# Kernel tuning notes

Measured on AMD Instinct MI355X. Metric: run time of the kernel, lower is better.

## Reference

```python
import jax, jax.numpy as jnp
import numpy as np

IN_F, OUT_F = 4096, 11008
MAXQ = 15  # 2**4 - 1 for wbits=4


def setup_inputs() -> dict:
    key = jax.random.key(0)
    k1, k2, k3, k4, k5 = jax.random.split(key, 5)
    inp = jax.random.normal(k1, (4, 64, IN_F), dtype=jnp.float32)
    weight = jax.random.normal(k2, (OUT_F, IN_F), dtype=jnp.float32) * 0.02
    bias = jax.random.normal(k3, (OUT_F,), dtype=jnp.float32) * 0.02
    # per-channel asymmetric quant params (as Quantizer.find_params would produce)
    scale = jax.random.uniform(k4, (OUT_F, 1), dtype=jnp.float32) * 0.01 + 1e-4
    zero = jnp.round(jax.random.uniform(k5, (OUT_F, 1), dtype=jnp.float32) * MAXQ)
    return {"input": inp, "weight": weight, "bias": bias,
            "scale": scale, "zero": zero, "maxq": MAXQ}


def reference(input, weight, bias, scale, zero, maxq):
    # fake-quantize weight: q = clamp(round(w/scale) + zero, 0, maxq); w_dq = scale*(q - zero)
    q = jnp.clip(jnp.round(weight / scale) + zero, 0.0, float(maxq))
    w_dq = scale * (q - zero)                      # [out, in]
    # F.linear: input @ w_dq.T + bias
    out = jnp.einsum('bsi,oi->bso', input, w_dq) + bias
    return out
```

## Files before the change

kernel.cpp:

```cpp
#include <hip/hip_runtime.h>
#include <stdint.h>

#define K_TOT 4096
#define N_TOT 11008
#define M_TOT 256
#define BM 128
#define BN 64
#define WST 72

using bf16x8 = __attribute__((ext_vector_type(8))) short;
using f32x4  = __attribute__((ext_vector_type(4))) float;

#define BAR() do {                                          \
    asm volatile("s_waitcnt lgkmcnt(0)" ::: "memory");      \
    __builtin_amdgcn_s_barrier();                           \
    asm volatile("" ::: "memory");                          \
} while (0)

__global__ void cvt_a_bf16(const float* __restrict__ in, uint32_t* __restrict__ out) {
    int i = blockIdx.x * blockDim.x + threadIdx.x;
    const float4 v = ((const float4*)in)[i];
    uint32_t a = __float_as_uint(v.x), b = __float_as_uint(v.y),
             c = __float_as_uint(v.z), d = __float_as_uint(v.w);
    a += 0x7FFFu + ((a >> 16) & 1u);
    b += 0x7FFFu + ((b >> 16) & 1u);
    c += 0x7FFFu + ((c >> 16) & 1u);
    d += 0x7FFFu + ((d >> 16) & 1u);
    uint2 o;
    o.x = (a >> 16) | (b & 0xFFFF0000u);
    o.y = (c >> 16) | (d & 0xFFFF0000u);
    ((uint2*)out)[i] = o;
}

__device__ __forceinline__ uint32_t pack_hi16(uint32_t u0, uint32_t u1) {
#if __has_builtin(__builtin_amdgcn_perm)
    return __builtin_amdgcn_perm(u1, u0, 0x07060302u);
#else
    return (u0 >> 16) | (u1 & 0xFFFF0000u);
#endif
}

__device__ __forceinline__ float clamp3(float q, float lo, float hi) {
#if __has_builtin(__builtin_amdgcn_fmed3f)
    return __builtin_amdgcn_fmed3f(q, lo, hi);
#else
    return fminf(fmaxf(q, lo), hi);
#endif
}

__device__ __forceinline__ void dequant16(const f32x4* w, float rs, float lo, float hi,
                                          float sc, uint32_t o[8]) {
    uint32_t u[16];
#pragma unroll
    for (int j = 0; j < 4; ++j) {
#pragma unroll
        for (int e = 0; e < 4; ++e) {
            float q  = rintf(w[j][e] * rs);
            q        = clamp3(q, lo, hi);
            float dq = q * sc;
            uint32_t b = __float_as_uint(dq);
            u[4 * j + e] = b + 0x7FFFu + ((b >> 16) & 1u);
        }
    }
#pragma unroll
    for (int i = 0; i < 8; ++i) o[i] = pack_hi16(u[2 * i], u[2 * i + 1]);
}

__global__ __launch_bounds__(256, 3)
void wql_gemm(const uint16_t* __restrict__ A,
              const float* __restrict__ W,
              const float* __restrict__ scale,
              const float* __restrict__ zero,
              float* __restrict__ P,
              int kloc) {
    __shared__ uint16_t sW[2][BN][WST];

    const int tid  = threadIdx.x;
    const int lane = tid & 63;
    const int wv   = tid >> 6;
    const int wm   = (wv & 1) * 64;
    const int wn   = (wv >> 1) * 32;
    const int m0   = blockIdx.x * BM;
    const int n0   = blockIdx.y * BN;
    const int k0   = blockIdx.z * kloc;
    const int nkt  = kloc >> 6;

    const int nloc = tid >> 2;
    const int kseg = tid & 3;
    const int wrow = n0 + nloc;
    const float* Wp = W + (size_t)wrow * K_TOT + k0 + kseg * 16;
    const float sc = scale[wrow];
    const float zp = zero[wrow];
    const float rs = 1.0f / sc;
    const float lo = -zp, hi = 15.0f - zp;

    const uint16_t* Ap[4];
#pragma unroll
    for (int mi = 0; mi < 4; ++mi)
        Ap[mi] = A + (size_t)(m0 + wm + mi * 16 + (lane & 15)) * K_TOT + k0 + (lane >> 4) * 8;

    f32x4 acc[4][2];
#pragma unroll
    for (int mi = 0; mi < 4; ++mi)
#pragma unroll
        for (int ni = 0; ni < 2; ++ni)
            acc[mi][ni] = (f32x4){0.f, 0.f, 0.f, 0.f};

    f32x4 bank[4][4];

#pragma unroll
    for (int s = 0; s < 3; ++s) {
        const f32x4* p = (const f32x4*)(Wp + (size_t)s * 64);
#pragma unroll
        for (int j = 0; j < 4; ++j) bank[s][j] = __builtin_nontemporal_load(p + j);
    }
    {
        uint32_t o[8];
        dequant16(bank[0], rs, lo, hi, sc, o);
        uint16_t* d = &sW[0][nloc][kseg * 16];
        ((uint4*)d)[0] = make_uint4(o[0], o[1], o[2], o[3]);
        ((uint4*)d)[1] = make_uint4(o[4], o[5], o[6], o[7]);
    }
    BAR();

    for (int st = 0; st < nkt; st += 4) {
#pragma unroll
        for (int u = 0; u < 4; ++u) {
            const int step = st + u;

            if (step + 3 < nkt) {
                const f32x4* p = (const f32x4*)(Wp + (size_t)(step + 3) * 64);
#pragma unroll
                for (int j = 0; j < 4; ++j)
                    bank[(u + 3) & 3][j] = __builtin_nontemporal_load(p + j);
            }

            {
                const int koff = step * 64;
#pragma unroll
                for (int s = 0; s < 2; ++s) {
                    bf16x8 a[4], b[2];
#pragma unroll
                    for (int mi = 0; mi < 4; ++mi)
                        a[mi] = *(const bf16x8*)(Ap[mi] + koff + s * 32);
#pragma unroll
                    for (int ni = 0; ni < 2; ++ni)
                        b[ni] = *(const bf16x8*)&sW[u & 1][wn + ni * 16 + (lane & 15)]
                                                  [s * 32 + (lane >> 4) * 8];
#pragma unroll
                    for (int mi = 0; mi < 4; ++mi)
#pragma unroll
                        for (int ni = 0; ni < 2; ++ni)
                            acc[mi][ni] = __builtin_amdgcn_mfma_f32_16x16x32_bf16(
                                a[mi], b[ni], acc[mi][ni], 0, 0, 0);
                }
            }

            if (step + 1 < nkt) {
                uint32_t o[8];
                dequant16(bank[(u + 1) & 3], rs, lo, hi, sc, o);
                uint16_t* d = &sW[(u + 1) & 1][nloc][kseg * 16];
                ((uint4*)d)[0] = make_uint4(o[0], o[1], o[2], o[3]);
                ((uint4*)d)[1] = make_uint4(o[4], o[5], o[6], o[7]);
            }

            BAR();
        }
    }

    float* Pb = P + (size_t)blockIdx.z * M_TOT * N_TOT;
    const int colbase = n0 + wn + (lane & 15);
    const int rbase = m0 + wm + ((lane >> 4) << 2);
#pragma unroll
    for (int mi = 0; mi < 4; ++mi) {
#pragma unroll
        for (int ni = 0; ni < 2; ++ni) {
            const int col = colbase + ni * 16;
#pragma unroll
            for (int r = 0; r < 4; ++r) {
                const int row = rbase + mi * 16 + r;
                __builtin_nontemporal_store(acc[mi][ni][r], &Pb[(size_t)row * N_TOT + col]);
            }
        }
    }
}

__global__ void reduce_bias(const float* __restrict__ P, const float* __restrict__ bias,
                            float* __restrict__ out, int ks) {
    const int i4 = blockIdx.x * blockDim.x + threadIdx.x;
    const size_t tot4 = (size_t)M_TOT * N_TOT / 4;
    const int col = (int)(((size_t)i4 * 4) % N_TOT);
    f32x4 acc = __builtin_nontemporal_load((const f32x4*)P + i4);
    for (int s = 1; s < ks; ++s) {
        const f32x4 v = __builtin_nontemporal_load((const f32x4*)P + (size_t)s * tot4 + i4);
        acc += v;
    }
    const float4 b = *(const float4*)(bias + col);
    acc[0] += b.x; acc[1] += b.y; acc[2] += b.z; acc[3] += b.w;
    *((f32x4*)out + i4) = acc;
}

extern "C" void kernel_launch(void* const* d_in, const int* in_sizes, int n_in,
                              void* d_out, int out_size, void* d_ws, size_t ws_size,
                              hipStream_t stream) {
    const float* inp    = (const float*)d_in[0];
    const float* weight = (const float*)d_in[1];
    const float* bias   = (const float*)d_in[2];
    const float* scale  = (const float*)d_in[3];
    const float* zero   = (const float*)d_in[4];

    const size_t A_BYTES = (size_t)M_TOT * K_TOT * 2;
    const size_t SLICE   = (size_t)M_TOT * N_TOT * 4;

    uint32_t* Abf = (uint32_t*)d_ws;
    float* partial;
    int KS;
    if (ws_size >= A_BYTES + 4 * SLICE) { KS = 4; partial = (float*)((char*)d_ws + A_BYTES); }
    else if (ws_size >= A_BYTES + 2 * SLICE) { KS = 2; partial = (float*)((char*)d_ws + A_BYTES); }
    else { KS = 1; partial = (float*)d_out; }

    cvt_a_bf16<<<dim3((M_TOT * K_TOT / 4) / 256), dim3(256), 0, stream>>>(inp, Abf);

    dim3 grid(M_TOT / BM, N_TOT / BN, KS);
    wql_gemm<<<grid, dim3(256), 0, stream>>>((const uint16_t*)Abf, weight, scale, zero,
                                             partial, K_TOT / KS);

    reduce_bias<<<dim3((M_TOT * N_TOT / 4) / 256), dim3(256), 0, stream>>>(
        partial, bias, (float*)d_out, KS);
}
```

Baseline: 407.7 us.

## Double-buffer A fragments in registers and drop nontemporal loads/stores

Prefetches the next k-step's bf16 A fragments into a double-buffered register array ahead of the MFMA loop, using sched_barrier to keep the prefetch ordered before compute. Weight bank loads, partial-sum stores and reduce loads switch from nontemporal to ordinary accesses, which may let the partials stay in cache between the GEMM and the reduction. This raises register pressure (an extra 16 bf16x8 registers) and could hurt occupancy at the 3-blocks-per-CU launch bound.

Result: slower. 435.9 us (+6.9%).

```diff
diff --git a/kernel.cpp b/kernel.cpp
--- a/kernel.cpp
+++ b/kernel.cpp
@@ -106,21 +106,31 @@
         for (int ni = 0; ni < 2; ++ni)
             acc[mi][ni] = (f32x4){0.f, 0.f, 0.f, 0.f};
 
-    f32x4 bank[4][4];
-
-#pragma unroll
-    for (int s = 0; s < 3; ++s) {
-        const f32x4* p = (const f32x4*)(Wp + (size_t)s * 64);
-#pragma unroll
-        for (int j = 0; j < 4; ++j) bank[s][j] = __builtin_nontemporal_load(p + j);
-    }
+    f32x4  bank[4][4];
+    bf16x8 ar[2][4][2];
+
     {
+        const f32x4* p = (const f32x4*)Wp;
+#pragma unroll
+        for (int j = 0; j < 4; ++j) bank[0][j] = p[j];
         uint32_t o[8];
         dequant16(bank[0], rs, lo, hi, sc, o);
         uint16_t* d = &sW[0][nloc][kseg * 16];
         ((uint4*)d)[0] = make_uint4(o[0], o[1], o[2], o[3]);
         ((uint4*)d)[1] = make_uint4(o[4], o[5], o[6], o[7]);
     }
+#pragma unroll
+    for (int mi = 0; mi < 4; ++mi)
+#pragma unroll
+        for (int s = 0; s < 2; ++s)
+            ar[0][mi][s] = *(const bf16x8*)(Ap[mi] + s * 32);
+    __builtin_amdgcn_sched_barrier(0);
+#pragma unroll
+    for (int ps = 1; ps <= 2; ++ps) {
+        const f32x4* p = (const f32x4*)(Wp + (size_t)ps * 64);
+#pragma unroll
+        for (int j = 0; j < 4; ++j) bank[ps][j] = p[j];
+    }
     BAR();
 
     for (int st = 0; st < nkt; st += 4) {
@@ -128,21 +138,27 @@
         for (int u = 0; u < 4; ++u) {
             const int step = st + u;
 
+            if (step + 1 < nkt) {
+                const int koff = (step + 1) * 64;
+#pragma unroll
+                for (int mi = 0; mi < 4; ++mi)
+#pragma unroll
+                    for (int s = 0; s < 2; ++s)
+                        ar[(u + 1) & 1][mi][s] = *(const bf16x8*)(Ap[mi] + koff + s * 32);
+            }
+            __builtin_amdgcn_sched_barrier(0);
+
             if (step + 3 < nkt) {
                 const f32x4* p = (const f32x4*)(Wp + (size_t)(step + 3) * 64);
 #pragma unroll
-                for (int j = 0; j < 4; ++j)
-                    bank[(u + 3) & 3][j] = __builtin_nontemporal_load(p + j);
-            }
+                for (int j = 0; j < 4; ++j) bank[(u + 3) & 3][j] = p[j];
+            }
+            __builtin_amdgcn_sched_barrier(0);
 
             {
-                const int koff = step * 64;
 #pragma unroll
                 for (int s = 0; s < 2; ++s) {
-                    bf16x8 a[4], b[2];
-#pragma unroll
-                    for (int mi = 0; mi < 4; ++mi)
-                        a[mi] = *(const bf16x8*)(Ap[mi] + koff + s * 32);
+                    bf16x8 b[2];
 #pragma unroll
                     for (int ni = 0; ni < 2; ++ni)
                         b[ni] = *(const bf16x8*)&sW[u & 1][wn + ni * 16 + (lane & 15)]
@@ -152,7 +168,7 @@
 #pragma unroll
                         for (int ni = 0; ni < 2; ++ni)
                             acc[mi][ni] = __builtin_amdgcn_mfma_f32_16x16x32_bf16(
-                                a[mi], b[ni], acc[mi][ni], 0, 0, 0);
+                                ar[u & 1][mi][s], b[ni], acc[mi][ni], 0, 0, 0);
                 }
             }
 
@@ -179,7 +195,7 @@
 #pragma unroll
             for (int r = 0; r < 4; ++r) {
                 const int row = rbase + mi * 16 + r;
-                __builtin_nontemporal_store(acc[mi][ni][r], &Pb[(size_t)row * N_TOT + col]);
+                Pb[(size_t)row * N_TOT + col] = acc[mi][ni][r];
             }
         }
     }
@@ -190,14 +206,14 @@
     const int i4 = blockIdx.x * blockDim.x + threadIdx.x;
     const size_t tot4 = (size_t)M_TOT * N_TOT / 4;
     const int col = (int)(((size_t)i4 * 4) % N_TOT);
-    f32x4 acc = __builtin_nontemporal_load((const f32x4*)P + i4);
+    float4 acc = ((const float4*)P)[i4];
     for (int s = 1; s < ks; ++s) {
-        const f32x4 v = __builtin_nontemporal_load((const f32x4*)P + (size_t)s * tot4 + i4);
-        acc += v;
+        const float4 v = ((const float4*)P)[(size_t)s * tot4 + i4];
+        acc.x += v.x; acc.y += v.y; acc.z += v.z; acc.w += v.w;
     }
     const float4 b = *(const float4*)(bias + col);
-    acc[0] += b.x; acc[1] += b.y; acc[2] += b.z; acc[3] += b.w;
-    *((f32x4*)out + i4) = acc;
+    acc.x += b.x; acc.y += b.y; acc.z += b.z; acc.w += b.w;
+    ((float4*)out)[i4] = acc;
 }
 
 extern "C" void kernel_launch(void* const* d_in, const int* in_sizes, int n_in,
```

## Restructure GEMM main loop with two-bank weight prefetch and sched barriers

Applied to the files above, without the earlier changes.

Reworks the main loop from a 4-deep register bank of weight prefetches into a 2-bank ping-pong macro with explicit sched_barriers. All A-fragment loads are hoisted ahead of the weight prefetch, and the MFMA order is interleaved with the B LDS reads. Nontemporal loads and stores are also replaced with ordinary ones in the GEMM epilogue and the reduction. The goal is lower register pressure and a more controlled instruction order, at the cost of a shallower prefetch distance that may expose more global load latency.

Result: faster. 340.4 us (-16.5%).

```diff
diff --git a/kernel.cpp b/kernel.cpp
--- a/kernel.cpp
+++ b/kernel.cpp
@@ -16,6 +16,8 @@
     __builtin_amdgcn_s_barrier();                           \
     asm volatile("" ::: "memory");                          \
 } while (0)
+
+#define MFMA(A, B, C) __builtin_amdgcn_mfma_f32_16x16x32_bf16((A), (B), (C), 0, 0, 0)
 
 __global__ void cvt_a_bf16(const float* __restrict__ in, uint32_t* __restrict__ out) {
     int i = blockIdx.x * blockDim.x + threadIdx.x;
@@ -66,6 +68,59 @@
     for (int i = 0; i < 8; ++i) o[i] = pack_hi16(u[2 * i], u[2 * i + 1]);
 }
 
+#define ITER(STEP, CUR, NXT, P) do {                                            \
+    const int _s = (STEP);                                                      \
+    const int _koff = _s * 64;                                                  \
+              \
+    bf16x8 a0 = *(const bf16x8*)(Ap0 + _koff),                                  \
+           a1 = *(const bf16x8*)(Ap0 + _koff + 32),                             \
+           a2 = *(const bf16x8*)(Ap1 + _koff),                                  \
+           a3 = *(const bf16x8*)(Ap1 + _koff + 32),                             \
+           a4 = *(const bf16x8*)(Ap2 + _koff),                                  \
+           a5 = *(const bf16x8*)(Ap2 + _koff + 32),                             \
+           a6 = *(const bf16x8*)(Ap3 + _koff),                                  \
+           a7 = *(const bf16x8*)(Ap3 + _koff + 32);                             \
+    __builtin_amdgcn_sched_barrier(0);                                          \
+     \
+    if (_s + 2 < nkt) {                                                         \
+        const f32x4* _p = (const f32x4*)(Wp + (size_t)(_s + 2) * 64);           \
+        CUR[0] = _p[0]; CUR[1] = _p[1]; CUR[2] = _p[2]; CUR[3] = _p[3];         \
+    }                                                                           \
+    __builtin_amdgcn_sched_barrier(0);                                          \
+                                    \
+    {                                                                           \
+        bf16x8 b00 = *(const bf16x8*)&sW[P][wn +      (lane & 15)][(lane >> 4) * 8]; \
+        bf16x8 b01 = *(const bf16x8*)&sW[P][wn + 16 + (lane & 15)][(lane >> 4) * 8]; \
+        acc[0][0] = MFMA(a0, b00, acc[0][0]);                                   \
+        acc[0][1] = MFMA(a0, b01, acc[0][1]);                                   \
+        acc[1][0] = MFMA(a2, b00, acc[1][0]);                                   \
+        acc[1][1] = MFMA(a2, b01, acc[1][1]);                                   \
+        acc[2][0] = MFMA(a4, b00, acc[2][0]);                                   \
+        acc[2][1] = MFMA(a4, b01, acc[2][1]);                                   \
+        acc[3][0] = MFMA(a6, b00, acc[3][0]);                                   \
+        acc[3][1] = MFMA(a6, b01, acc[3][1]);                                   \
+        bf16x8 b10 = *(const bf16x8*)&sW[P][wn +      (lane & 15)][32 + (lane >> 4) * 8]; \
+        bf16x8 b11 = *(const bf16x8*)&sW[P][wn + 16 + (lane & 15)][32 + (lane >> 4) * 8]; \
+        acc[0][0] = MFMA(a1, b10, acc[0][0]);                                   \
+        acc[0][1] = MFMA(a1, b11, acc[0][1]);                                   \
+        acc[1][0] = MFMA(a3, b10, acc[1][0]);                                   \
+        acc[1][1] = MFMA(a3, b11, acc[1][1]);                                   \
+        acc[2][0] = MFMA(a5, b10, acc[2][0]);                                   \
+        acc[2][1] = MFMA(a5, b11, acc[2][1]);                                   \
+        acc[3][0] = MFMA(a7, b10, acc[3][0]);                                   \
+        acc[3][1] = MFMA(a7, b11, acc[3][1]);                                   \
+    }                                                                           \
+                     \
+    if (_s + 1 < nkt) {                                                         \
+        uint32_t o[8];                                                          \
+        dequant16(NXT, rs, lo, hi, sc, o);                                      \
+        uint16_t* _d = &sW[P ^ 1][nloc][kseg * 16];                             \
+        ((uint4*)_d)[0] = make_uint4(o[0], o[1], o[2], o[3]);                   \
+        ((uint4*)_d)[1] = make_uint4(o[4], o[5], o[6], o[7]);                   \
+    }                                                                           \
+    BAR();                                                                      \
+} while (0)
+
 __global__ __launch_bounds__(256, 3)
 void wql_gemm(const uint16_t* __restrict__ A,
               const float* __restrict__ W,
@@ -94,10 +149,10 @@
     const float rs = 1.0f / sc;
     const float lo = -zp, hi = 15.0f - zp;
 
-    const uint16_t* Ap[4];
-#pragma unroll
-    for (int mi = 0; mi < 4; ++mi)
-        Ap[mi] = A + (size_t)(m0 + wm + mi * 16 + (lane & 15)) * K_TOT + k0 + (lane >> 4) * 8;
+    const uint16_t* Ap0 = A + (size_t)(m0 + wm +  0 + (lane & 15)) * K_TOT + k0 + (lane >> 4) * 8;
+    const uint16_t* Ap1 = A + (size_t)(m0 + wm + 16 + (lane & 15)) * K_TOT + k0 + (lane >> 4) * 8;
+    const uint16_t* Ap2 = A + (size_t)(m0 + wm + 32 + (lane & 15)) * K_TOT + k0 + (lane >> 4) * 8;
+    const uint16_t* Ap3 = A + (size_t)(m0 + wm + 48 + (lane & 15)) * K_TOT + k0 + (lane >> 4) * 8;
 
     f32x4 acc[4][2];
 #pragma unroll
@@ -106,66 +161,27 @@
         for (int ni = 0; ni < 2; ++ni)
             acc[mi][ni] = (f32x4){0.f, 0.f, 0.f, 0.f};
 
-    f32x4 bank[4][4];
-
-#pragma unroll
-    for (int s = 0; s < 3; ++s) {
-        const f32x4* p = (const f32x4*)(Wp + (size_t)s * 64);
-#pragma unroll
-        for (int j = 0; j < 4; ++j) bank[s][j] = __builtin_nontemporal_load(p + j);
-    }
+    f32x4 bank0[4], bank1[4];
+
+    {
+        const f32x4* p0 = (const f32x4*)Wp;
+        bank0[0] = p0[0]; bank0[1] = p0[1]; bank0[2] = p0[2]; bank0[3] = p0[3];
+        const f32x4* p1 = (const f32x4*)(Wp + 64);
+        bank1[0] = p1[0]; bank1[1] = p1[1]; bank1[2] = p1[2]; bank1[3] = p1[3];
+    }
+    __builtin_amdgcn_sched_barrier(0);
     {
         uint32_t o[8];
-        dequant16(bank[0], rs, lo, hi, sc, o);
+        dequant16(bank0, rs, lo, hi, sc, o);
         uint16_t* d = &sW[0][nloc][kseg * 16];
         ((uint4*)d)[0] = make_uint4(o[0], o[1], o[2], o[3]);
         ((uint4*)d)[1] = make_uint4(o[4], o[5], o[6], o[7]);
     }
     BAR();
 
-    for (int st = 0; st < nkt; st += 4) {
-#pragma unroll
-        for (int u = 0; u < 4; ++u) {
-            const int step = st + u;
-
-            if (step + 3 < nkt) {
-                const f32x4* p = (const f32x4*)(Wp + (size_t)(step + 3) * 64);
-#pragma unroll
-                for (int j = 0; j < 4; ++j)
-                    bank[(u + 3) & 3][j] = __builtin_nontemporal_load(p + j);
-            }
-
-            {
-                const int koff = step * 64;
-#pragma unroll
-                for (int s = 0; s < 2; ++s) {
-                    bf16x8 a[4], b[2];
-#pragma unroll
-                    for (int mi = 0; mi < 4; ++mi)
-                        a[mi] = *(const bf16x8*)(Ap[mi] + koff + s * 32);
-#pragma unroll
-                    for (int ni = 0; ni < 2; ++ni)
-                        b[ni] = *(const bf16x8*)&sW[u & 1][wn + ni * 16 + (lane & 15)]
-                                                  [s * 32 + (lane >> 4) * 8];
-#pragma unroll
-                    for (int mi = 0; mi < 4; ++mi)
-#pragma unroll
-                        for (int ni = 0; ni < 2; ++ni)
-                            acc[mi][ni] = __builtin_amdgcn_mfma_f32_16x16x32_bf16(
-                                a[mi], b[ni], acc[mi][ni], 0, 0, 0);
-                }
-            }
-
-            if (step + 1 < nkt) {
-                uint32_t o[8];
-                dequant16(bank[(u + 1) & 3], rs, lo, hi, sc, o);
-                uint16_t* d = &sW[(u + 1) & 1][nloc][kseg * 16];
-                ((uint4*)d)[0] = make_uint4(o[0], o[1], o[2], o[3]);
-                ((uint4*)d)[1] = make_uint4(o[4], o[5], o[6], o[7]);
-            }
-
-            BAR();
-        }
+    for (int s = 0; s < nkt; s += 2) {
+        ITER(s,     bank0, bank1, 0);
+        ITER(s + 1, bank1, bank0, 1);
     }
 
     float* Pb = P + (size_t)blockIdx.z * M_TOT * N_TOT;
@@ -179,7 +195,7 @@
 #pragma unroll
             for (int r = 0; r < 4; ++r) {
                 const int row = rbase + mi * 16 + r;
-                __builtin_nontemporal_store(acc[mi][ni][r], &Pb[(size_t)row * N_TOT + col]);
+                Pb[(size_t)row * N_TOT + col] = acc[mi][ni][r];
             }
         }
     }
@@ -190,14 +206,14 @@
     const int i4 = blockIdx.x * blockDim.x + threadIdx.x;
     const size_t tot4 = (size_t)M_TOT * N_TOT / 4;
     const int col = (int)(((size_t)i4 * 4) % N_TOT);
-    f32x4 acc = __builtin_nontemporal_load((const f32x4*)P + i4);
+    float4 acc = ((const float4*)P)[i4];
     for (int s = 1; s < ks; ++s) {
-        const f32x4 v = __builtin_nontemporal_load((const f32x4*)P + (size_t)s * tot4 + i4);
-        acc += v;
+        const float4 v = ((const float4*)P)[(size_t)s * tot4 + i4];
+        acc.x += v.x; acc.y += v.y; acc.z += v.z; acc.w += v.w;
     }
     const float4 b = *(const float4*)(bias + col);
-    acc[0] += b.x; acc[1] += b.y; acc[2] += b.z; acc[3] += b.w;
-    *((f32x4*)out + i4) = acc;
+    acc.x += b.x; acc.y += b.y; acc.z += b.z; acc.w += b.w;
+    ((float4*)out)[i4] = acc;
 }
 
 extern "C" void kernel_launch(void* const* d_in, const int* in_sizes, int n_in,
```
